# Performance work log

Measured on AMD Instinct MI355X. Metric: run time of the kernel, lower is better.

Reference implementation:

```python
import jax, jax.numpy as jnp
import numpy as np
from jax import lax

ROUTING_ITERS = 3
CLASSES = 10
CAPS_DIM = 8
N_CAPS = 32 * 6 * 6  # 1152
DN = ('NCHW', 'OIHW', 'NCHW')


def setup_inputs() -> dict:
    key = jax.random.key(0)
    k1, k2, k3, k4 = jax.random.split(key, 4)
    x = jax.random.normal(k1, (256, 1, 28, 28), dtype=jnp.float32)
    conv1_w = jax.random.normal(k2, (256, 1, 9, 9), dtype=jnp.float32) * 0.05
    conv1_b = jnp.zeros((256,), dtype=jnp.float32)
    conv2_w = jax.random.normal(k3, (256, 256, 9, 9), dtype=jnp.float32) * 0.01
    conv2_b = jnp.zeros((256,), dtype=jnp.float32)
    # torch.randn init, as in the original Parameter
    W = jax.random.normal(k4, (CLASSES, N_CAPS, 16, CAPS_DIM), dtype=jnp.float32)
    return {"x": x, "conv1_w": conv1_w, "conv1_b": conv1_b,
            "conv2_w": conv2_w, "conv2_b": conv2_b, "W": W}


def _squash_primary(t):
    # module-level squash: scale = norm^2/(1+norm^2), NO division by norm
    sq = jnp.sum(t * t, axis=-1, keepdims=True)
    return (sq / (1.0 + sq)) * t


def _squash_routing(t):
    # CapsNet.squash: scale = sq/(1+sq) * t / sqrt(sq)
    sq = jnp.sum(t * t, axis=-1, keepdims=True)
    return (sq / (1.0 + sq)) * t / jnp.sqrt(sq)


def reference(x, conv1_w, conv1_b, conv2_w, conv2_b, W):
    B = x.shape[0]
    h = lax.conv_general_dilated(x, conv1_w, (1, 1), 'VALID', dimension_numbers=DN)
    h = h + conv1_b[None, :, None, None]
    h = jax.nn.relu(h)                    # [B,256,20,20]
    h = lax.conv_general_dilated(h, conv2_w, (2, 2), 'VALID', dimension_numbers=DN)
    h = h + conv2_b[None, :, None, None]  # [B,256,6,6]
    u = h.reshape(B, -1, CAPS_DIM)        # [B,1152,8]
    u = _squash_primary(u)
    xp = jnp.transpose(u, (1, 2, 0))      # [1152,8,B]
    # broadcasted matmul: [C,1152,16,8] @ [1152,8,B] -> [C,1152,16,B]
    u_hat = jnp.einsum('cnij,njb->cnib', W, xp)
    b = jnp.zeros_like(u_hat)
    outputs = None
    for i in range(ROUTING_ITERS):
        probs = jax.nn.softmax(b, axis=1)               # over the 1152 capsules
        s = jnp.sum(probs * u_hat, axis=1, keepdims=True)  # [C,1,16,B]
        outputs = _squash_routing(s)                    # squash over last (batch) axis
        if i != ROUTING_ITERS - 1:
            delta_b = jnp.sum(u_hat * outputs, axis=-1, keepdims=True)
            b = b + delta_b
    out = jnp.squeeze(outputs, axis=1)    # [C,16,B]
    out = jnp.transpose(out, (2, 0, 1))   # [B,C,16]
    return jnp.sum(out * out, axis=2)     # [B,C]
```

## Files before the change

kernel.cpp:

```cpp
#include <hip/hip_runtime.h>
#include <math.h>

using short8 = __attribute__((ext_vector_type(8))) short;
using f32x16 = __attribute__((ext_vector_type(16))) float;

static const size_t B_QHI = 0;
static const size_t B_QLO = 47316992;
static const size_t B_WHI = 94633984;
static const size_t B_WLO = 105250816;
static const size_t B_H2  = 115867648;
static const size_t B_H2B = 125304832;
static const size_t B_END_SPLIT = 134742016;
static const size_t B_UH  = 0;
static const size_t B_OB  = 94633984;

__device__ __forceinline__ unsigned short bf16_rne(float v) {
    unsigned int u = __builtin_bit_cast(unsigned int, v);
    u += 0x7FFFu + ((u >> 16) & 1u);
    return (unsigned short)(u >> 16);
}
__device__ __forceinline__ float bf16_tof(unsigned short h) {
    unsigned int u = ((unsigned int)h) << 16;
    return __builtin_bit_cast(float, u);
}

__global__ __launch_bounds__(256) void conv1_kernel(
        const float* __restrict__ x, const float* __restrict__ w1,
        const float* __restrict__ b1,
        unsigned short* __restrict__ qhi, unsigned short* __restrict__ qlo) {
    int b  = blockIdx.x;
    int xh = blockIdx.y;
    int c  = threadIdx.x;
    __shared__ float xs[28][20];
    for (int i = c; i < 560; i += 256) {
        int row = i / 20, cl = i - row * 20, gc = xh * 10 + cl;
        xs[row][cl] = (gc < 28) ? x[(size_t)b*784 + row*28 + gc] : 0.f;
    }
    float wr[81];
    #pragma unroll
    for (int k = 0; k < 81; ++k) wr[k] = w1[c*81 + k];
    float bias = b1[c];
    __syncthreads();
    for (int oy = 0; oy < 19; ++oy) {
        float acc[12];
        #pragma unroll
        for (int e = 0; e < 12; ++e) acc[e] = 0.f;
        #pragma unroll
        for (int ky = 0; ky < 9; ++ky) {
            float xr[20];
            #pragma unroll
            for (int i = 0; i < 20; ++i) xr[i] = xs[oy + ky][i];
            #pragma unroll
            for (int kx = 0; kx < 9; ++kx) {
                float wv_ = wr[ky*9 + kx];
                #pragma unroll
                for (int e = 0; e < 12; ++e)
                    acc[e] = fmaf(xr[e + kx], wv_, acc[e]);
            }
        }
        #pragma unroll
        for (int e = 0; e < 12; ++e) {
            int ox = xh*10 + e;
            if (e < 10 && ox < 19) {
                float v = fmaxf(bias + acc[e], 0.f);
                unsigned short hi = bf16_rne(v);
                unsigned short lo = bf16_rne(v - bf16_tof(hi));
                size_t o = ((size_t)((oy*19 + ox)*16 + (c >> 4))*256 + b)*16 + (c & 15);
                qhi[o] = hi; qlo[o] = lo;
            }
        }
    }
}

__global__ __launch_bounds__(256) void w2t_kernel(
        const float* __restrict__ w2,
        unsigned short* __restrict__ whi, unsigned short* __restrict__ wlo) {
    int c    = blockIdx.x;
    int half = blockIdx.y;
    int t = threadIdx.x;
    __shared__ float buf[128*81];
    const float* src = w2 + (size_t)c*20736 + (size_t)half*128*81;
    for (int i = t; i < 128*81; i += 256) buf[i] = src[i];
    __syncthreads();
    int kk = t >> 7, cil = t & 127;
    int ci = half*128 + cil;
    size_t cbase = ((size_t)(c >> 5)*16 + (ci >> 4))*32 + (c & 31);
    for (int k2 = 0; k2 < 41; ++k2) {
        int k = k2*2 + kk;
        if (k < 81) {
            float v = buf[cil*81 + k];
            unsigned short hi = bf16_rne(v);
            unsigned short lo = bf16_rne(v - bf16_tof(hi));
            size_t o = (((size_t)k*4096 + cbase)*16) + (ci & 15);
            whi[o] = hi; wlo[o] = lo;
        }
    }
}

__global__ __launch_bounds__(512) void conv2_mfma(
        const unsigned short* __restrict__ qhi, const unsigned short* __restrict__ qlo,
        const unsigned short* __restrict__ whi, const unsigned short* __restrict__ wlo,
        const float* __restrict__ b2, float* __restrict__ h2t) {
    int blk = blockIdx.x;
    int bt  = blk & 7;
    int rest = blk >> 3;
    int kh = rest & 1;  rest >>= 1;
    int cg = rest & 7;
    int oy = rest >> 3;
    int t = threadIdx.x;
    int wv = t >> 6, l = t & 63;
    int cis = kh*8 + wv;

    int loff = (l & 31)*16 + (l >> 5)*8;

    f32x16 acc[6];
    #pragma unroll
    for (int i = 0; i < 6; ++i)
        #pragma unroll
        for (int r = 0; r < 16; ++r) acc[i][r] = 0.f;

    #pragma unroll 1
    for (int ky = 0; ky < 9; ++ky) {
        int qy = oy*2 + ky;
        short8 afh[19], afl[19], bfh[9], bfl[9];
        size_t abase = (((size_t)(qy*19)*16 + cis)*256)*16 + (size_t)bt*512 + loff;
        #pragma unroll
        for (int q = 0; q < 19; ++q) {
            afh[q] = *(const short8*)(qhi + abase + (size_t)q*65536);
            afl[q] = *(const short8*)(qlo + abase + (size_t)q*65536);
        }
        size_t bbase = (((size_t)(ky*9)*8 + cg)*16 + cis)*512 + loff;
        #pragma unroll
        for (int kx = 0; kx < 9; ++kx) {
            bfh[kx] = *(const short8*)(whi + bbase + (size_t)kx*65536);
            bfl[kx] = *(const short8*)(wlo + bbase + (size_t)kx*65536);
        }
        #pragma unroll
        for (int kx = 0; kx < 9; ++kx) {
            #pragma unroll
            for (int oxl = 0; oxl < 6; ++oxl) {
                int q = 2*oxl + kx;
                acc[oxl] = __builtin_amdgcn_mfma_f32_32x32x16_bf16(afh[q], bfh[kx], acc[oxl], 0, 0, 0);
                acc[oxl] = __builtin_amdgcn_mfma_f32_32x32x16_bf16(afh[q], bfl[kx], acc[oxl], 0, 0, 0);
                acc[oxl] = __builtin_amdgcn_mfma_f32_32x32x16_bf16(afl[q], bfh[kx], acc[oxl], 0, 0, 0);
            }
        }
    }

    float* hp = h2t + (size_t)kh * 2359296;
    __shared__ float buf[4][3][16][64];
    #define REDUCE_STORE(A0, POFF)                                              \
    {                                                                           \
        if (wv < 4) {                                                           \
            _Pragma("unroll")                                                   \
            for (int i = 0; i < 3; ++i)                                         \
                _Pragma("unroll")                                               \
                for (int r = 0; r < 16; ++r) buf[wv][i][r][l] = acc[(A0)+i][r]; \
        }                                                                       \
        __syncthreads();                                                        \
        if (wv >= 4) {                                                          \
            _Pragma("unroll")                                                   \
            for (int i = 0; i < 3; ++i)                                         \
                _Pragma("unroll")                                               \
                for (int r = 0; r < 16; ++r) buf[wv-4][i][r][l] += acc[(A0)+i][r]; \
        }                                                                       \
        __syncthreads();                                                        \
        float* ebuf = &buf[0][0][0][0];                                         \
        if (wv == 0) {                                                          \
            float bv = (kh == 0) ? b2[cg*32 + (l & 31)] : 0.f;                  \
            float vals[3][16];                                                  \
            _Pragma("unroll")                                                   \
            for (int i = 0; i < 3; ++i)                                         \
                _Pragma("unroll")                                               \
                for (int r = 0; r < 16; ++r)                                    \
                    vals[i][r] = buf[0][i][r][l] + buf[1][i][r][l]              \
                               + buf[2][i][r][l] + buf[3][i][r][l] + bv;        \
            _Pragma("unroll")                                                   \
            for (int i = 0; i < 3; ++i)                                         \
                _Pragma("unroll")                                               \
                for (int r = 0; r < 16; ++r) {                                  \
                    int row = (r & 3) + 8*(r >> 2) + 4*(l >> 5);                \
                    ebuf[i*1056 + row*33 + (l & 31)] = vals[i][r];              \
                }                                                               \
        }                                                                       \
        __syncthreads();                                                        \
        _Pragma("unroll 1")                                                     \
        for (int pass = 0; pass < 6; ++pass) {                                  \
            int row_id = pass*16 + (t >> 5);                                    \
            int oxl = row_id >> 5, c = row_id & 31;                             \
            float v = ebuf[oxl*1056 + (t & 31)*33 + c];                         \
            int p = oy*6 + (POFF) + oxl;                                        \
            hp[(size_t)((cg*32 + c)*36 + p)*256 + bt*32 + (t & 31)] = v;        \
        }                                                                       \
        __syncthreads();                                                        \
    }
    REDUCE_STORE(0, 0)
    REDUCE_STORE(3, 3)
    #undef REDUCE_STORE
}

__global__ __launch_bounds__(256) void uhat_kernel(
        const float* __restrict__ h2t, const float* __restrict__ h2t2,
        const float* __restrict__ W, unsigned short* __restrict__ uhat) {
    int ch = blockIdx.x;
    int c  = blockIdx.y;
    int t  = threadIdx.x;
    __shared__ float Wl[2048];
    const float* wsrc = W + ((size_t)c*1152 + ch*16)*128;
    for (int i = t; i < 2048; i += 256) Wl[i] = wsrc[i];
    __syncthreads();
    #pragma unroll 1
    for (int nn = 0; nn < 16; ++nn) {
        int n = ch*16 + nn;
        float v[8]; float sq = 0.f;
        #pragma unroll
        for (int j = 0; j < 8; ++j) {
            size_t idx = (size_t)(n*8 + j)*256 + t;
            v[j] = h2t[idx] + h2t2[idx];
            sq = fmaf(v[j], v[j], sq);
        }
        float sc = sq / (1.0f + sq);
        #pragma unroll
        for (int j = 0; j < 8; ++j) v[j] *= sc;
        #pragma unroll
        for (int i = 0; i < 16; ++i) {
            float uh = 0.f;
            #pragma unroll
            for (int j = 0; j < 8; ++j)
                uh = fmaf(Wl[(nn*16 + i)*8 + j], v[j], uh);
            uhat[((size_t)(c*16 + i)*1152 + n)*256 + t] = bf16_rne(uh);
        }
    }
}

__global__ __launch_bounds__(512) void rout_kernel(
        const unsigned short* __restrict__ uhat, float* __restrict__ ob) {
    int ci = blockIdx.x;
    int t  = threadIdx.x;
    int wv = t >> 6, l = t & 63;
    const unsigned short* U = uhat + (size_t)ci*1152*256;
    __shared__ float bsum[1152];
    __shared__ float p[1152];
    __shared__ float outb[256];
    __shared__ float sred[16][256];
    __shared__ float red[8];
    for (int k = t; k < 1152; k += 512) bsum[k] = 0.f;
    __syncthreads();

    #pragma unroll 1
    for (int it = 0; it < 3; ++it) {
        float lv[3];
        float m = -1e30f;
        #pragma unroll
        for (int k = 0; k < 3; ++k) {
            int n = t + k*512;
            lv[k] = (n < 1152) ? bsum[n] : -1e30f;
            m = fmaxf(m, lv[k]);
        }
        #pragma unroll
        for (int mm = 1; mm < 64; mm <<= 1) m = fmaxf(m, __shfl_xor(m, mm, 64));
        if (l == 0) red[wv] = m;
        __syncthreads();
        m = red[0];
        #pragma unroll
        for (int k = 1; k < 8; ++k) m = fmaxf(m, red[k]);
        __syncthreads();
        float se = 0.f;
        #pragma unroll
        for (int k = 0; k < 3; ++k) {
            int n = t + k*512;
            if (n < 1152) {
                float e = expf(lv[k] - m);
                p[n] = e;
                se += e;
            }
        }
        #pragma unroll
        for (int mm = 1; mm < 64; mm <<= 1) se += __shfl_xor(se, mm, 64);
        if (l == 0) red[wv] = se;
        __syncthreads();
        se = red[0];
        #pragma unroll
        for (int k = 1; k < 8; ++k) se += red[k];
        float inv = 1.0f / se;
        #pragma unroll
        for (int k = 0; k < 3; ++k) {
            int n = t + k*512;
            if (n < 1152) p[n] *= inv;
        }
        __syncthreads();

        {
            int ng = t >> 5, bo = t & 31;
            float s8[8];
            #pragma unroll
            for (int e = 0; e < 8; ++e) s8[e] = 0.f;
            int n0 = ng * 72;
            #pragma unroll 4
            for (int nn = 0; nn < 72; ++nn) {
                int n = n0 + nn;
                float pv = p[n];
                short8 u8 = *(const short8*)(U + (size_t)n*256 + bo*8);
                #pragma unroll
                for (int e = 0; e < 8; ++e)
                    s8[e] = fmaf(pv, bf16_tof((unsigned short)u8[e]), s8[e]);
            }
            #pragma unroll
            for (int e = 0; e < 8; ++e) sred[ng][bo*8 + e] = s8[e];
        }
        __syncthreads();

        float s = 0.f;
        if (t < 256) {
            #pragma unroll
            for (int g = 0; g < 16; ++g) s += sred[g][t];
            float v2 = s * s;
            #pragma unroll
            for (int mm = 1; mm < 64; mm <<= 1) v2 += __shfl_xor(v2, mm, 64);
            if ((t & 63) == 0) red[t >> 6] = v2;
        }
        __syncthreads();
        float total = red[0] + red[1] + red[2] + red[3];
        if (t < 256) {
            float scq = total / ((1.0f + total) * sqrtf(total));
            float o = scq * s;
            if (it == 2) ob[(size_t)ci*256 + t] = o;
            else outb[t] = o;
        }
        if (it == 2) break;
        __syncthreads();

        {
            int nl = l >> 5, bo = l & 31;
            #pragma unroll 2
            for (int pass = 0; pass < 72; ++pass) {
                int n = pass*16 + wv*2 + nl;
                short8 u8 = *(const short8*)(U + (size_t)n*256 + bo*8);
                float d = 0.f;
                #pragma unroll
                for (int e = 0; e < 8; ++e)
                    d = fmaf(bf16_tof((unsigned short)u8[e]), outb[bo*8 + e], d);
                #pragma unroll
                for (int mm = 1; mm < 32; mm <<= 1) d += __shfl_xor(d, mm, 64);
                if (bo == 0) bsum[n] += d;
            }
        }
        __syncthreads();
    }
}

__global__ __launch_bounds__(256) void final_kernel(
        const float* __restrict__ obuf, float* __restrict__ out) {
    int c = blockIdx.x;
    int t = threadIdx.x;
    float s = 0.0f;
    #pragma unroll
    for (int i = 0; i < 16; ++i) {
        float v = obuf[((size_t)c*16 + i)*256 + t];
        s = fmaf(v, v, s);
    }
    out[(size_t)t*10 + c] = s;
}

extern "C" void kernel_launch(void* const* d_in, const int* in_sizes, int n_in,
                              void* d_out, int out_size, void* d_ws, size_t ws_size,
                              hipStream_t stream) {
    const float* x  = (const float*)d_in[0];
    const float* w1 = (const float*)d_in[1];
    const float* b1 = (const float*)d_in[2];
    const float* w2 = (const float*)d_in[3];
    const float* b2 = (const float*)d_in[4];
    const float* W  = (const float*)d_in[5];
    float* out = (float*)d_out;
    (void)in_sizes; (void)n_in; (void)out_size;

    if (ws_size < B_END_SPLIT) return;

    char* wsb = (char*)d_ws;
    unsigned short* qhi = (unsigned short*)(wsb + B_QHI);
    unsigned short* qlo = (unsigned short*)(wsb + B_QLO);
    unsigned short* whi = (unsigned short*)(wsb + B_WHI);
    unsigned short* wlo = (unsigned short*)(wsb + B_WLO);
    float* h2t  = (float*)(wsb + B_H2);
    float* h2t2 = (float*)(wsb + B_H2B);
    unsigned short* uh = (unsigned short*)(wsb + B_UH);
    float* ob = (float*)(wsb + B_OB);

    w2t_kernel<<<dim3(256, 2), 256, 0, stream>>>(w2, whi, wlo);
    conv1_kernel<<<dim3(256, 2), 256, 0, stream>>>(x, w1, b1, qhi, qlo);
    conv2_mfma<<<768, 512, 0, stream>>>(qhi, qlo, whi, wlo, b2, h2t);
    uhat_kernel<<<dim3(72, 10), 256, 0, stream>>>(h2t, h2t2, W, uh);
    rout_kernel<<<160, 512, 0, stream>>>(uh, ob);
    final_kernel<<<10, 256, 0, stream>>>(ob, out);
}
```

Measured before the change: 532.4 us.

## Precompute uniform-softmax first routing iteration via column sums; merge conv1 and w2 prep kernels

In the first routing iteration the softmax is uniform (1/1152), so s is just the mean of u_hat over capsules. The uhat kernel now also writes per-chunk partial column sums, and the routing kernel reduces these instead of streaming all of u_hat for the weighted sum in iteration 0. The conv1 and weight-transpose kernels are merged into one launch, and some unroll factors are raised. The trade-off is an extra 72-way partial-sum buffer read with strided access, plus extra register pressure in uhat.

```diff
diff --git a/kernel.cpp b/kernel.cpp
--- a/kernel.cpp
+++ b/kernel.cpp
@@ -13,6 +13,7 @@
 static const size_t B_END_SPLIT = 134742016;
 static const size_t B_UH  = 0;
 static const size_t B_OB  = 94633984;
+static const size_t B_CP  = 94797824;
 
 __device__ __forceinline__ unsigned short bf16_rne(float v) {
     unsigned int u = __builtin_bit_cast(unsigned int, v);
@@ -24,75 +25,74 @@
     return __builtin_bit_cast(float, u);
 }
 
-__global__ __launch_bounds__(256) void conv1_kernel(
+__global__ __launch_bounds__(256) void prep_kernel(
         const float* __restrict__ x, const float* __restrict__ w1,
-        const float* __restrict__ b1,
-        unsigned short* __restrict__ qhi, unsigned short* __restrict__ qlo) {
-    int b  = blockIdx.x;
-    int xh = blockIdx.y;
-    int c  = threadIdx.x;
-    __shared__ float xs[28][20];
-    for (int i = c; i < 560; i += 256) {
-        int row = i / 20, cl = i - row * 20, gc = xh * 10 + cl;
-        xs[row][cl] = (gc < 28) ? x[(size_t)b*784 + row*28 + gc] : 0.f;
-    }
-    float wr[81];
-    #pragma unroll
-    for (int k = 0; k < 81; ++k) wr[k] = w1[c*81 + k];
-    float bias = b1[c];
-    __syncthreads();
-    for (int oy = 0; oy < 19; ++oy) {
-        float acc[12];
-        #pragma unroll
-        for (int e = 0; e < 12; ++e) acc[e] = 0.f;
-        #pragma unroll
-        for (int ky = 0; ky < 9; ++ky) {
-            float xr[20];
-            #pragma unroll
-            for (int i = 0; i < 20; ++i) xr[i] = xs[oy + ky][i];
-            #pragma unroll
-            for (int kx = 0; kx < 9; ++kx) {
-                float wv_ = wr[ky*9 + kx];
+        const float* __restrict__ b1, const float* __restrict__ w2,
+        unsigned short* __restrict__ qhi, unsigned short* __restrict__ qlo,
+        unsigned short* __restrict__ whi, unsigned short* __restrict__ wlo) {
+    __shared__ float sh[10368];
+    int blk = blockIdx.x;
+    int t = threadIdx.x;
+    if (blk < 512) {
+        int b = blk >> 1, xh = blk & 1, c = t;
+        float (*xs)[20] = (float(*)[20])sh;
+        for (int i = c; i < 560; i += 256) {
+            int row = i / 20, cl = i - row * 20, gc = xh * 10 + cl;
+            xs[row][cl] = (gc < 28) ? x[(size_t)b*784 + row*28 + gc] : 0.f;
+        }
+        float wr[81];
+        #pragma unroll
+        for (int k = 0; k < 81; ++k) wr[k] = w1[c*81 + k];
+        float bias = b1[c];
+        __syncthreads();
+        for (int oy = 0; oy < 19; ++oy) {
+            float acc[12];
+            #pragma unroll
+            for (int e = 0; e < 12; ++e) acc[e] = 0.f;
+            #pragma unroll
+            for (int ky = 0; ky < 9; ++ky) {
+                float xr[20];
                 #pragma unroll
-                for (int e = 0; e < 12; ++e)
-                    acc[e] = fmaf(xr[e + kx], wv_, acc[e]);
-            }
-        }
-        #pragma unroll
-        for (int e = 0; e < 12; ++e) {
-            int ox = xh*10 + e;
-            if (e < 10 && ox < 19) {
-                float v = fmaxf(bias + acc[e], 0.f);
+                for (int i = 0; i < 20; ++i) xr[i] = xs[oy + ky][i];
+                #pragma unroll
+                for (int kx = 0; kx < 9; ++kx) {
+                    float wv_ = wr[ky*9 + kx];
+                    #pragma unroll
+                    for (int e = 0; e < 12; ++e)
+                        acc[e] = fmaf(xr[e + kx], wv_, acc[e]);
+                }
+            }
+            #pragma unroll
+            for (int e = 0; e < 12; ++e) {
+                int ox = xh*10 + e;
+                if (e < 10 && ox < 19) {
+                    float v = fmaxf(bias + acc[e], 0.f);
+                    unsigned short hi = bf16_rne(v);
+                    unsigned short lo = bf16_rne(v - bf16_tof(hi));
+                    size_t o = ((size_t)((oy*19 + ox)*16 + (c >> 4))*256 + b)*16 + (c & 15);
+                    qhi[o] = hi; qlo[o] = lo;
+                }
+            }
+        }
+    } else {
+        int idx = blk - 512;
+        int c = idx >> 1, half = idx & 1;
+        float* buf = sh;
+        const float* src = w2 + (size_t)c*20736 + (size_t)half*128*81;
+        for (int i = t; i < 128*81; i += 256) buf[i] = src[i];
+        __syncthreads();
+        int kk = t >> 7, cil = t & 127;
+        int ci = half*128 + cil;
+        size_t cbase = ((size_t)(c >> 5)*16 + (ci >> 4))*32 + (c & 31);
+        for (int k2 = 0; k2 < 41; ++k2) {
+            int k = k2*2 + kk;
+            if (k < 81) {
+                float v = buf[cil*81 + k];
                 unsigned short hi = bf16_rne(v);
                 unsigned short lo = bf16_rne(v - bf16_tof(hi));
-                size_t o = ((size_t)((oy*19 + ox)*16 + (c >> 4))*256 + b)*16 + (c & 15);
-                qhi[o] = hi; qlo[o] = lo;
-            }
-        }
-    }
-}
-
-__global__ __launch_bounds__(256) void w2t_kernel(
-        const float* __restrict__ w2,
-        unsigned short* __restrict__ whi, unsigned short* __restrict__ wlo) {
-    int c    = blockIdx.x;
-    int half = blockIdx.y;
-    int t = threadIdx.x;
-    __shared__ float buf[128*81];
-    const float* src = w2 + (size_t)c*20736 + (size_t)half*128*81;
-    for (int i = t; i < 128*81; i += 256) buf[i] = src[i];
-    __syncthreads();
-    int kk = t >> 7, cil = t & 127;
-    int ci = half*128 + cil;
-    size_t cbase = ((size_t)(c >> 5)*16 + (ci >> 4))*32 + (c & 31);
-    for (int k2 = 0; k2 < 41; ++k2) {
-        int k = k2*2 + kk;
-        if (k < 81) {
-            float v = buf[cil*81 + k];
-            unsigned short hi = bf16_rne(v);
-            unsigned short lo = bf16_rne(v - bf16_tof(hi));
-            size_t o = (((size_t)k*4096 + cbase)*16) + (ci & 15);
-            whi[o] = hi; wlo[o] = lo;
+                size_t o = (((size_t)k*4096 + cbase)*16) + (ci & 15);
+                whi[o] = hi; wlo[o] = lo;
+            }
         }
     }
 }
@@ -201,7 +201,8 @@
 
 __global__ __launch_bounds__(256) void uhat_kernel(
         const float* __restrict__ h2t, const float* __restrict__ h2t2,
-        const float* __restrict__ W, unsigned short* __restrict__ uhat) {
+        const float* __restrict__ W, unsigned short* __restrict__ uhat,
+        float* __restrict__ colpart) {
     int ch = blockIdx.x;
     int c  = blockIdx.y;
     int t  = threadIdx.x;
@@ -209,6 +210,9 @@
     const float* wsrc = W + ((size_t)c*1152 + ch*16)*128;
     for (int i = t; i < 2048; i += 256) Wl[i] = wsrc[i];
     __syncthreads();
+    float cp[16];
+    #pragma unroll
+    for (int i = 0; i < 16; ++i) cp[i] = 0.f;
     #pragma unroll 1
     for (int nn = 0; nn < 16; ++nn) {
         int n = ch*16 + nn;
@@ -228,13 +232,19 @@
             #pragma unroll
             for (int j = 0; j < 8; ++j)
                 uh = fmaf(Wl[(nn*16 + i)*8 + j], v[j], uh);
-            uhat[((size_t)(c*16 + i)*1152 + n)*256 + t] = bf16_rne(uh);
-        }
-    }
+            unsigned short ub = bf16_rne(uh);
+            uhat[((size_t)(c*16 + i)*1152 + n)*256 + t] = ub;
+            cp[i] += bf16_tof(ub);
+        }
+    }
+    #pragma unroll
+    for (int i = 0; i < 16; ++i)
+        colpart[(size_t)ch*40960 + (size_t)(c*16 + i)*256 + t] = cp[i];
 }
 
 __global__ __launch_bounds__(512) void rout_kernel(
-        const unsigned short* __restrict__ uhat, float* __restrict__ ob) {
+        const unsigned short* __restrict__ uhat, const float* __restrict__ colpart,
+        float* __restrict__ ob) {
     int ci = blockIdx.x;
     int t  = threadIdx.x;
     int wv = t >> 6, l = t & 63;
@@ -247,8 +257,48 @@
     for (int k = t; k < 1152; k += 512) bsum[k] = 0.f;
     __syncthreads();
 
+    #define DELTA_PASS                                                          \
+    {                                                                           \
+        int nl = l >> 5, bo = l & 31;                                           \
+        _Pragma("unroll 4")                                                     \
+        for (int pass = 0; pass < 72; ++pass) {                                 \
+            int n = pass*16 + wv*2 + nl;                                        \
+            short8 u8 = *(const short8*)(U + (size_t)n*256 + bo*8);             \
+            float d = 0.f;                                                      \
+            _Pragma("unroll")                                                   \
+            for (int e = 0; e < 8; ++e)                                         \
+                d = fmaf(bf16_tof((unsigned short)u8[e]), outb[bo*8 + e], d);   \
+            _Pragma("unroll")                                                   \
+            for (int mm = 1; mm < 32; mm <<= 1) d += __shfl_xor(d, mm, 64);     \
+            if (bo == 0) bsum[n] += d;                                          \
+        }                                                                       \
+    }
+
+    {
+        float s = 0.f;
+        if (t < 256) {
+            const float* cp = colpart + (size_t)ci*256 + t;
+            #pragma unroll 8
+            for (int ch = 0; ch < 72; ++ch) s += cp[(size_t)ch*40960];
+            s *= (1.0f / 1152.0f);
+        }
+        float v2 = s * s;
+        #pragma unroll
+        for (int mm = 1; mm < 64; mm <<= 1) v2 += __shfl_xor(v2, mm, 64);
+        if (t < 256 && l == 0) red[wv] = v2;
+        __syncthreads();
+        float total = red[0] + red[1] + red[2] + red[3];
+        if (t < 256) {
+            float scq = total / ((1.0f + total) * sqrtf(total));
+            outb[t] = scq * s;
+        }
+        __syncthreads();
+        DELTA_PASS
+        __syncthreads();
+    }
+
     #pragma unroll 1
-    for (int it = 0; it < 3; ++it) {
+    for (int it = 1; it < 3; ++it) {
         float lv[3];
         float m = -1e30f;
         #pragma unroll
@@ -296,7 +346,7 @@
             #pragma unroll
             for (int e = 0; e < 8; ++e) s8[e] = 0.f;
             int n0 = ng * 72;
-            #pragma unroll 4
+            #pragma unroll 8
             for (int nn = 0; nn < 72; ++nn) {
                 int n = n0 + nn;
                 float pv = p[n];
@@ -329,24 +379,10 @@
         }
         if (it == 2) break;
         __syncthreads();
-
-        {
-            int nl = l >> 5, bo = l & 31;
-            #pragma unroll 2
-            for (int pass = 0; pass < 72; ++pass) {
-                int n = pass*16 + wv*2 + nl;
-                short8 u8 = *(const short8*)(U + (size_t)n*256 + bo*8);
-                float d = 0.f;
-                #pragma unroll
-                for (int e = 0; e < 8; ++e)
-                    d = fmaf(bf16_tof((unsigned short)u8[e]), outb[bo*8 + e], d);
-                #pragma unroll
-                for (int mm = 1; mm < 32; mm <<= 1) d += __shfl_xor(d, mm, 64);
-                if (bo == 0) bsum[n] += d;
-            }
-        }
-        __syncthreads();
-    }
+        DELTA_PASS
+        __syncthreads();
+    }
+    #undef DELTA_PASS
 }
 
 __global__ __launch_bounds__(256) void final_kernel(
@@ -385,11 +421,11 @@
     float* h2t2 = (float*)(wsb + B_H2B);
     unsigned short* uh = (unsigned short*)(wsb + B_UH);
     float* ob = (float*)(wsb + B_OB);
-
-    w2t_kernel<<<dim3(256, 2), 256, 0, stream>>>(w2, whi, wlo);
-    conv1_kernel<<<dim3(256, 2), 256, 0, stream>>>(x, w1, b1, qhi, qlo);
+    float* cp = (float*)(wsb + B_CP);
+
+    prep_kernel<<<1024, 256, 0, stream>>>(x, w1, b1, w2, qhi, qlo, whi, wlo);
     conv2_mfma<<<768, 512, 0, stream>>>(qhi, qlo, whi, wlo, b2, h2t);
-    uhat_kernel<<<dim3(72, 10), 256, 0, stream>>>(h2t, h2t2, W, uh);
-    rout_kernel<<<160, 512, 0, stream>>>(uh, ob);
+    uhat_kernel<<<dim3(72, 10), 256, 0, stream>>>(h2t, h2t2, W, uh, cp);
+    rout_kernel<<<160, 512, 0, stream>>>(uh, cp, ob);
     final_kernel<<<10, 256, 0, stream>>>(ob, out);
 }
```

Measured after the change: 466.7 us. 1.14x faster.
